# Kernel tuning notes

Hardware: AMD Instinct MI355X
Metric: run time of the kernel (lower is better)

## Reference

```python
import jax, jax.numpy as jnp
import numpy as np

DIM = 768
HEADS = 12
HEAD_DIM = DIM // HEADS
MLP_DIM = 4 * DIM
EPS = 1e-5


def setup_inputs() -> dict:
    key = jax.random.key(0)
    ks = jax.random.split(key, 8)
    s = lambda fan_in: 1.0 / np.sqrt(fan_in)
    return {
        "x": jax.random.normal(ks[0], (2, 2048, DIM), dtype=jnp.float32),
        "ln1_w": jnp.ones((DIM,), jnp.float32),
        "ln1_b": jnp.zeros((DIM,), jnp.float32),
        # weights stored [in, out]
        "qkv_w": jax.random.normal(ks[1], (DIM, 3 * DIM), jnp.float32) * s(DIM),
        "qkv_b": jnp.zeros((3 * DIM,), jnp.float32),
        "proj_w": jax.random.normal(ks[2], (DIM, DIM), jnp.float32) * s(DIM),
        "proj_b": jnp.zeros((DIM,), jnp.float32),
        "ln2_w": jnp.ones((DIM,), jnp.float32),
        "ln2_b": jnp.zeros((DIM,), jnp.float32),
        "lin1_w": jax.random.normal(ks[3], (DIM, MLP_DIM), jnp.float32) * s(DIM),
        "lin1_b": jnp.zeros((MLP_DIM,), jnp.float32),
        "lin2_w": jax.random.normal(ks[4], (MLP_DIM, DIM), jnp.float32) * s(MLP_DIM),
        "lin2_b": jnp.zeros((DIM,), jnp.float32),
    }


def _layernorm(x, w, b):
    mu = jnp.mean(x, axis=-1, keepdims=True)
    var = jnp.mean(jnp.square(x - mu), axis=-1, keepdims=True)
    return (x - mu) * jax.lax.rsqrt(var + EPS) * w + b


def _attention(x, qkv_w, qkv_b, proj_w, proj_b):
    B, N, C = x.shape
    qkv = (x @ qkv_w + qkv_b).reshape(B, N, 3, HEADS, HEAD_DIM)
    q, k, v = qkv[:, :, 0], qkv[:, :, 1], qkv[:, :, 2]  # [B, N, H, Dh]
    scale = HEAD_DIM ** -0.5
    attn = jnp.einsum("bqhd,bkhd->bhqk", q, k) * scale  # full NxN scores
    attn = jax.nn.softmax(attn, axis=-1)
    out = jnp.einsum("bhqk,bkhd->bqhd", attn, v).reshape(B, N, C)
    return out @ proj_w + proj_b


def reference(x, ln1_w, ln1_b, qkv_w, qkv_b, proj_w, proj_b,
              ln2_w, ln2_b, lin1_w, lin1_b, lin2_w, lin2_b):
    x = x + _attention(_layernorm(x, ln1_w, ln1_b), qkv_w, qkv_b, proj_w, proj_b)
    h = _layernorm(x, ln2_w, ln2_b)
    h = jax.nn.gelu(h @ lin1_w + lin1_b, approximate=False) @ lin2_w + lin2_b
    return x + h
```

## Files before the change

kernel.cpp:

```cpp
#include <hip/hip_runtime.h>
#include <hip/hip_bf16.h>
#include <math.h>

#define DIM 768
#define NTOK 4096
#define SEQ 2048
#define HEADS 12
#define HD 64

using bf16x8 = __attribute__((ext_vector_type(8))) __bf16;
using f32x4  = __attribute__((ext_vector_type(4))) float;
typedef unsigned short u16;

__device__ inline u16 f2bf(float f) {
  union { float f; unsigned u; } v; v.f = f;
  unsigned r = v.u + 0x7fffu + ((v.u >> 16) & 1u);
  return (u16)(r >> 16);
}

__device__ inline void pk2bf(float a, float b, u16* o0, u16* o1) {
  union { __hip_bfloat162 h; u16 u[2]; } cv;
  cv.h = __float22bfloat162_rn(make_float2(a, b));
  *o0 = cv.u[0];
  *o1 = cv.u[1];
}

__device__ inline unsigned pku32(float a, float b) {
  union { __hip_bfloat162 h; unsigned u; } cv;
  cv.h = __float22bfloat162_rn(make_float2(a, b));
  return cv.u;
}

__device__ inline void plane32_swap(unsigned &a, unsigned &b) {
  asm("v_permlane32_swap_b32 %0, %1" : "+v"(a), "+v"(b));
}
__device__ inline void plane16_swap(unsigned &a, unsigned &b) {
  asm("v_permlane16_swap_b32 %0, %1" : "+v"(a), "+v"(b));
}

__device__ inline float gelu_t(float x) {
  float z = x * (1.5957691216f + 0.0713548162f * x * x);
  return x / (1.0f + __expf(-z));
}

__device__ inline void gl_lds16(const u16* g, u16* l) {
  __builtin_amdgcn_global_load_lds(
      (const __attribute__((address_space(1))) unsigned int*)g,
      (__attribute__((address_space(3))) unsigned int*)l, 16, 0, 0);
}

__global__ __launch_bounds__(256) void ln_kernel(const float* __restrict__ x,
                                                 const float* __restrict__ w,
                                                 const float* __restrict__ b,
                                                 u16* __restrict__ y) {
  int row = blockIdx.x;
  int t = threadIdx.x;
  const float* xr = x + (size_t)row * DIM;
  float v0 = xr[t], v1 = xr[t + 256], v2 = xr[t + 512];
  float s = v0 + v1 + v2;
  float q = v0 * v0 + v1 * v1 + v2 * v2;
  for (int o = 32; o > 0; o >>= 1) {
    s += __shfl_down(s, o, 64);
    q += __shfl_down(q, o, 64);
  }
  __shared__ float ws_[4], wq_[4], mb[2];
  int wid = t >> 6;
  if ((t & 63) == 0) { ws_[wid] = s; wq_[wid] = q; }
  __syncthreads();
  if (t == 0) {
    float S = ws_[0] + ws_[1] + ws_[2] + ws_[3];
    float Q = wq_[0] + wq_[1] + wq_[2] + wq_[3];
    float mean = S * (1.0f / DIM);
    float var = Q * (1.0f / DIM) - mean * mean;
    mb[0] = mean;
    mb[1] = rsqrtf(var + 1e-5f);
  }
  __syncthreads();
  float mean = mb[0], rstd = mb[1];
  u16* yr = y + (size_t)row * DIM;
  yr[t]       = f2bf((v0 - mean) * rstd * w[t]       + b[t]);
  yr[t + 256] = f2bf((v1 - mean) * rstd * w[t + 256] + b[t + 256]);
  yr[t + 512] = f2bf((v2 - mean) * rstd * w[t + 512] + b[t + 512]);
}

__global__ __launch_bounds__(256) void redln_kernel(
    const float* __restrict__ P0, const float* __restrict__ P1,
    const float* __restrict__ bias, const float* __restrict__ res,
    float* __restrict__ x2, const float* __restrict__ lnw,
    const float* __restrict__ lnb, u16* __restrict__ y) {
  int row = blockIdx.x;
  int t = threadIdx.x;
  size_t off = (size_t)row * DIM;
  float v[3];
#pragma unroll
  for (int k = 0; k < 3; ++k) {
    int c = t + k * 256;
    v[k] = P0[off + c] + P1[off + c] + bias[c] + res[off + c];
    x2[off + c] = v[k];
  }
  float s = v[0] + v[1] + v[2];
  float q = v[0] * v[0] + v[1] * v[1] + v[2] * v[2];
  for (int o = 32; o > 0; o >>= 1) {
    s += __shfl_down(s, o, 64);
    q += __shfl_down(q, o, 64);
  }
  __shared__ float ws_[4], wq_[4], mb[2];
  int wid = t >> 6;
  if ((t & 63) == 0) { ws_[wid] = s; wq_[wid] = q; }
  __syncthreads();
  if (t == 0) {
    float S = ws_[0] + ws_[1] + ws_[2] + ws_[3];
    float Q = wq_[0] + wq_[1] + wq_[2] + wq_[3];
    float mean = S * (1.0f / DIM);
    float var = Q * (1.0f / DIM) - mean * mean;
    mb[0] = mean;
    mb[1] = rsqrtf(var + 1e-5f);
  }
  __syncthreads();
  float mean = mb[0], rstd = mb[1];
#pragma unroll
  for (int k = 0; k < 3; ++k) {
    int c = t + k * 256;
    y[off + c] = f2bf((v[k] - mean) * rstd * lnw[c] + lnb[c]);
  }
}

__global__ __launch_bounds__(256) void wcvt_all(
    const float* __restrict__ W0, const float* __restrict__ W1,
    const float* __restrict__ W2, const float* __restrict__ W3,
    u16* __restrict__ T0, u16* __restrict__ T1,
    u16* __restrict__ T2, u16* __restrict__ T3) {
  int id = blockIdx.x;
  const float* W; u16* Wt; int K, N, local;
  if (id < 1728)      { W = W0; Wt = T0; K = 768;  N = 2304; local = id; }
  else if (id < 2304) { W = W1; Wt = T1; K = 768;  N = 768;  local = id - 1728; }
  else if (id < 4608) { W = W2; Wt = T2; K = 768;  N = 3072; local = id - 2304; }
  else                { W = W3; Wt = T3; K = 3072; N = 768;  local = id - 4608; }
  int ntiles = N / 32;
  int n0 = (local % ntiles) * 32, k0 = (local / ntiles) * 32;
  __shared__ float tile[32][33];
  int tid = threadIdx.x;
  int c = tid & 31, r8 = tid >> 5;
#pragma unroll
  for (int p = 0; p < 4; ++p) {
    int k = r8 + p * 8;
    tile[k][c] = W[(size_t)(k0 + k) * N + n0 + c];
  }
  __syncthreads();
#pragma unroll
  for (int p = 0; p < 4; ++p) {
    int n = r8 + p * 8;
    Wt[(size_t)(n0 + n) * K + k0 + c] = f2bf(tile[c][n]);
  }
}

__global__ __launch_bounds__(256) void vtr_kernel(const u16* __restrict__ qkvB,
                                                  u16* __restrict__ vT) {
  __shared__ u16 tile[32][33];
  int v0 = blockIdx.x * 32, j0 = blockIdx.y * 32, b = blockIdx.z;
  int tid = threadIdx.x;
  int c = tid & 31, r8 = tid >> 5;
#pragma unroll
  for (int p = 0; p < 4; ++p) {
    int r = r8 + p * 8;
    tile[r][c] = qkvB[((size_t)(b * SEQ + j0 + r)) * 2304 + 1536 + v0 + c];
  }
  __syncthreads();
#pragma unroll
  for (int p = 0; p < 4; ++p) {
    int r = r8 + p * 8;
    vT[((size_t)(b * 768 + v0 + r)) * SEQ + j0 + c] = tile[c][r];
  }
}

__global__ __launch_bounds__(256) void bgemm_kernel(
    const u16* __restrict__ A, const u16* __restrict__ Bt,
    const float* __restrict__ bias, u16* __restrict__ Cb,
    int M, int N, int K, int act) {
  __shared__ __align__(16) u16 Asl[128 * 64];
  __shared__ __align__(16) u16 Bsl[128 * 64];
  int tid = threadIdx.x;
  int lane = tid & 63, wave = tid >> 6;
  int wm = wave >> 1, wn = wave & 1;
  int bm = blockIdx.y * 128, bn = blockIdx.x * 128;
  int l15 = lane & 15, quad = lane >> 4;
  int sm8 = tid >> 3;
  int kgx = (tid & 7) ^ (sm8 & 7);

  f32x4 acc[4][4] = {};
  const u16* Ap = A + (size_t)(bm + sm8) * K + kgx * 8;
  const u16* Bp = Bt + (size_t)(bn + sm8) * K + kgx * 8;
  u16* Al = &Asl[(wave * 8) * 64];
  u16* Bl = &Bsl[(wave * 8) * 64];
  int xr = l15 & 7;

  for (int k0 = 0; k0 < K; k0 += 64) {
#pragma unroll
    for (int p = 0; p < 4; ++p)
      gl_lds16(Ap + (size_t)(p * 32) * K + k0, Al + p * 32 * 64);
#pragma unroll
    for (int p = 0; p < 4; ++p)
      gl_lds16(Bp + (size_t)(p * 32) * K + k0, Bl + p * 32 * 64);
    __syncthreads();
#pragma unroll
    for (int ks = 0; ks < 2; ++ks) {
      int pu = ((ks << 2) + quad) ^ xr;
      bf16x8 af[4], bfr[4];
#pragma unroll
      for (int i = 0; i < 4; ++i) {
        af[i]  = *(const bf16x8*)&Asl[(wm * 64 + i * 16 + l15) * 64 + pu * 8];
        bfr[i] = *(const bf16x8*)&Bsl[(wn * 64 + i * 16 + l15) * 64 + pu * 8];
      }
#pragma unroll
      for (int i = 0; i < 4; ++i)
#pragma unroll
        for (int j = 0; j < 4; ++j)
          acc[i][j] = __builtin_amdgcn_mfma_f32_16x16x32_bf16(af[i], bfr[j], acc[i][j], 0, 0, 0);
    }
    __syncthreads();
  }

#pragma unroll
  for (int i = 0; i < 4; ++i) {
#pragma unroll
    for (int j = 0; j < 4; ++j) {
      int n = bn + wn * 64 + j * 16 + l15;
      float bv = bias[n];
      float val[4];
#pragma unroll
      for (int r = 0; r < 4; ++r) {
        float v = acc[i][j][r] + bv;
        val[r] = act ? gelu_t(v) : v;
      }
      u16 c0, c1, c2, c3;
      pk2bf(val[0], val[1], &c0, &c1);
      pk2bf(val[2], val[3], &c2, &c3);
      size_t mbase = (size_t)(bm + wm * 64 + i * 16 + quad * 4) * N + n;
      Cb[mbase]         = c0;
      Cb[mbase + N]     = c1;
      Cb[mbase + 2 * N] = c2;
      Cb[mbase + 3 * N] = c3;
    }
  }
}

__global__ __launch_bounds__(256) void bgemm_splitk(
    const u16* __restrict__ A, const u16* __restrict__ Bt,
    float* __restrict__ P0, float* __restrict__ P1,
    int M, int N, int K) {
  __shared__ __align__(16) u16 Asl[128 * 64];
  __shared__ __align__(16) u16 Bsl[64 * 64];
  int tid = threadIdx.x;
  int lane = tid & 63, wave = tid >> 6;
  int wm = wave >> 1, wn = wave & 1;
  int bm = blockIdx.y * 128, bn = blockIdx.x * 64;
  int l15 = lane & 15, quad = lane >> 4;
  int sm8 = tid >> 3;
  int kgx = (tid & 7) ^ (sm8 & 7);
  int half = K >> 1;
  int kbeg = blockIdx.z * half;

  f32x4 acc[4][2] = {};
  const u16* Ap = A + (size_t)(bm + sm8) * K + kbeg + kgx * 8;
  const u16* Bp = Bt + (size_t)(bn + sm8) * K + kbeg + kgx * 8;
  u16* Al = &Asl[(wave * 8) * 64];
  u16* Bl = &Bsl[(wave * 8) * 64];
  int xr = l15 & 7;

  for (int k0 = 0; k0 < half; k0 += 64) {
#pragma unroll
    for (int p = 0; p < 4; ++p)
      gl_lds16(Ap + (size_t)(p * 32) * K + k0, Al + p * 32 * 64);
#pragma unroll
    for (int p = 0; p < 2; ++p)
      gl_lds16(Bp + (size_t)(p * 32) * K + k0, Bl + p * 32 * 64);
    __syncthreads();
#pragma unroll
    for (int ks = 0; ks < 2; ++ks) {
      int pu = ((ks << 2) + quad) ^ xr;
      bf16x8 af[4], bfr[2];
#pragma unroll
      for (int i = 0; i < 4; ++i)
        af[i] = *(const bf16x8*)&Asl[(wm * 64 + i * 16 + l15) * 64 + pu * 8];
#pragma unroll
      for (int j = 0; j < 2; ++j)
        bfr[j] = *(const bf16x8*)&Bsl[(wn * 32 + j * 16 + l15) * 64 + pu * 8];
#pragma unroll
      for (int i = 0; i < 4; ++i)
#pragma unroll
        for (int j = 0; j < 2; ++j)
          acc[i][j] = __builtin_amdgcn_mfma_f32_16x16x32_bf16(af[i], bfr[j], acc[i][j], 0, 0, 0);
    }
    __syncthreads();
  }

  float* P = blockIdx.z ? P1 : P0;
#pragma unroll
  for (int i = 0; i < 4; ++i) {
#pragma unroll
    for (int j = 0; j < 2; ++j) {
      int n = bn + wn * 32 + j * 16 + l15;
#pragma unroll
      for (int r = 0; r < 4; ++r) {
        int m = bm + wm * 64 + i * 16 + quad * 4 + r;
        P[(size_t)m * N + n] = acc[i][j][r];
      }
    }
  }
}

__global__ __launch_bounds__(256) void red_kernel(
    const float* P0, const float* __restrict__ P1,
    const float* __restrict__ bias, const float* __restrict__ res,
    float* O, int Ncols) {
  int i = blockIdx.x * 256 + threadIdx.x;
  float4 a = ((const float4*)P0)[i];
  float4 b = ((const float4*)P1)[i];
  float4 r = ((const float4*)res)[i];
  int col = (i * 4) % Ncols;
  float4 bi = *(const float4*)&bias[col];
  float4 o;
  o.x = a.x + b.x + r.x + bi.x;
  o.y = a.y + b.y + r.y + bi.y;
  o.z = a.z + b.z + r.z + bi.z;
  o.w = a.w + b.w + r.w + bi.w;
  ((float4*)O)[i] = o;
}

__global__ __launch_bounds__(256) void attn_kernel(const u16* __restrict__ qkv,
                                                   const u16* __restrict__ vT,
                                                   u16* __restrict__ out) {
  __shared__ __align__(16) u16 Qs[64 * 64];
  __shared__ __align__(16) u16 Ks[2][64 * 64];
  __shared__ __align__(16) u16 Vs[2][64 * 64];

  int tid = threadIdx.x;
  int lane = tid & 63, wave = tid >> 6;
  int l15 = lane & 15, quad = lane >> 4;
  int qt = blockIdx.x * 64;
  int h = blockIdx.y, b = blockIdx.z;
  size_t base = (size_t)b * SEQ;
  int srow = lane >> 3;
  int sux = (lane & 7) ^ (srow & 7);
  int r0 = wave * 16;
  const u16* qbase = qkv + (base + qt) * 2304 + h * HD;
  const u16* kbase = qkv + base * 2304 + 768 + h * HD;
  const u16* vbase = vT + ((size_t)(b * HEADS + h) * HD) * SEQ;

  gl_lds16(qbase + (size_t)(r0 + srow) * 2304 + sux * 8, Qs + r0 * 64);
  gl_lds16(qbase + (size_t)(r0 + 8 + srow) * 2304 + sux * 8, Qs + (r0 + 8) * 64);
  gl_lds16(kbase + (size_t)(r0 + srow) * 2304 + sux * 8, Ks[0] + r0 * 64);
  gl_lds16(kbase + (size_t)(r0 + 8 + srow) * 2304 + sux * 8, Ks[0] + (r0 + 8) * 64);
  gl_lds16(vbase + (size_t)(r0 + srow) * SEQ + sux * 8, Vs[0] + r0 * 64);
  gl_lds16(vbase + (size_t)(r0 + 8 + srow) * SEQ + sux * 8, Vs[0] + (r0 + 8) * 64);
  __syncthreads();

  int xr = l15 & 7;
  bf16x8 aq0 = *(const bf16x8*)&Qs[(wave * 16 + l15) * 64 + ((quad ^ xr)) * 8];
  bf16x8 aq1 = *(const bf16x8*)&Qs[(wave * 16 + l15) * 64 + (((4 + quad) ^ xr)) * 8];

  f32x4 o_acc[4] = {};
  float lsum = 0.f;
  const float KEXP = 0.18033688011112042f;

  for (int t = 0; t < 32; ++t) {
    int buf = t & 1;
    if (t < 31) {
      size_t kt1 = (size_t)(t + 1) * 64;
      gl_lds16(kbase + (kt1 + r0 + srow) * 2304 + sux * 8, Ks[buf ^ 1] + r0 * 64);
      gl_lds16(kbase + (kt1 + r0 + 8 + srow) * 2304 + sux * 8, Ks[buf ^ 1] + (r0 + 8) * 64);
      gl_lds16(vbase + (size_t)(r0 + srow) * SEQ + kt1 + sux * 8, Vs[buf ^ 1] + r0 * 64);
      gl_lds16(vbase + (size_t)(r0 + 8 + srow) * SEQ + kt1 + sux * 8, Vs[buf ^ 1] + (r0 + 8) * 64);
    }

    f32x4 sT[4] = {};
    __builtin_amdgcn_s_setprio(1);
#pragma unroll
    for (int jt = 0; jt < 4; ++jt) {
      bf16x8 bk0 = *(const bf16x8*)&Ks[buf][(jt * 16 + l15) * 64 + ((quad ^ xr)) * 8];
      sT[jt] = __builtin_amdgcn_mfma_f32_16x16x32_bf16(bk0, aq0, sT[jt], 0, 0, 0);
      bf16x8 bk1 = *(const bf16x8*)&Ks[buf][(jt * 16 + l15) * 64 + (((4 + quad) ^ xr)) * 8];
      sT[jt] = __builtin_amdgcn_mfma_f32_16x16x32_bf16(bk1, aq1, sT[jt], 0, 0, 0);
    }
    __builtin_amdgcn_s_setprio(0);

    unsigned w01[4][2];
#pragma unroll
    for (int jt = 0; jt < 4; ++jt) {
      float p0 = __builtin_amdgcn_exp2f(sT[jt][0] * KEXP);
      float p1 = __builtin_amdgcn_exp2f(sT[jt][1] * KEXP);
      float p2 = __builtin_amdgcn_exp2f(sT[jt][2] * KEXP);
      float p3 = __builtin_amdgcn_exp2f(sT[jt][3] * KEXP);
      lsum += (p0 + p1) + (p2 + p3);
      w01[jt][0] = pku32(p0, p1);
      w01[jt][1] = pku32(p2, p3);
    }

    __builtin_amdgcn_s_setprio(1);
#pragma unroll
    for (int ks = 0; ks < 2; ++ks) {
      unsigned a0 = w01[2 * ks][0], b0 = w01[2 * ks + 1][0];
      plane32_swap(a0, b0);
      plane16_swap(a0, b0);
      unsigned a1 = w01[2 * ks][1], b1 = w01[2 * ks + 1][1];
      plane32_swap(a1, b1);
      plane16_swap(a1, b1);
      union { bf16x8 v; unsigned u[4]; } AP;
      AP.u[0] = a0; AP.u[1] = a1; AP.u[2] = b0; AP.u[3] = b1;
#pragma unroll
      for (int dt = 0; dt < 4; ++dt) {
        bf16x8 bv = *(const bf16x8*)&Vs[buf][(dt * 16 + l15) * 64 + (((ks << 2) + quad) ^ xr) * 8];
        o_acc[dt] = __builtin_amdgcn_mfma_f32_16x16x32_bf16(AP.v, bv, o_acc[dt], 0, 0, 0);
      }
    }
    __builtin_amdgcn_s_setprio(0);
    __syncthreads();
  }

  lsum += __shfl_xor(lsum, 16, 64);
  lsum += __shfl_xor(lsum, 32, 64);
  float linv = 1.0f / lsum;
  float lr[4];
#pragma unroll
  for (int r = 0; r < 4; ++r) lr[r] = __shfl(linv, quad * 4 + r, 64);

#pragma unroll
  for (int r = 0; r < 4; ++r) {
    size_t trow = (base + qt + wave * 16 + quad * 4 + r) * DIM + h * HD;
    u16 c0, c1, c2, c3;
    pk2bf(o_acc[0][r] * lr[r], o_acc[1][r] * lr[r], &c0, &c1);
    pk2bf(o_acc[2][r] * lr[r], o_acc[3][r] * lr[r], &c2, &c3);
    out[trow + 0 * 16 + l15] = c0;
    out[trow + 1 * 16 + l15] = c1;
    out[trow + 2 * 16 + l15] = c2;
    out[trow + 3 * 16 + l15] = c3;
  }
}

extern "C" void kernel_launch(void* const* d_in, const int* in_sizes, int n_in,
                              void* d_out, int out_size, void* d_ws, size_t ws_size,
                              hipStream_t stream) {
  const float* x     = (const float*)d_in[0];
  const float* ln1w  = (const float*)d_in[1];
  const float* ln1b  = (const float*)d_in[2];
  const float* qkvw  = (const float*)d_in[3];
  const float* qkvbi = (const float*)d_in[4];
  const float* projw = (const float*)d_in[5];
  const float* projb = (const float*)d_in[6];
  const float* ln2w  = (const float*)d_in[7];
  const float* ln2b  = (const float*)d_in[8];
  const float* l1w   = (const float*)d_in[9];
  const float* l1b   = (const float*)d_in[10];
  const float* l2w   = (const float*)d_in[11];
  const float* l2b   = (const float*)d_in[12];
  float* out = (float*)d_out;

  char* w = (char*)d_ws;
  u16*   h     = (u16*)w;   w += (size_t)NTOK * DIM * 2;
  u16*   qkvB  = (u16*)w;
  u16*   mid   = (u16*)w;   w += (size_t)NTOK * 3072 * 2;
  u16*   attnb = (u16*)w;   w += (size_t)NTOK * DIM * 2;
  float* x2    = (float*)w; w += (size_t)NTOK * DIM * 4;
  u16*   vTb   = (u16*)w;   w += (size_t)NTOK * DIM * 2;
  u16*   qkvwt = (u16*)w;   w += (size_t)DIM * 2304 * 2;
  u16*   projwt= (u16*)w;   w += (size_t)DIM * DIM * 2;
  u16*   l1wt  = (u16*)w;   w += (size_t)DIM * 3072 * 2;
  u16*   l2wt  = (u16*)w;   w += (size_t)3072 * DIM * 2;
  float* Pbuf  = (float*)w; w += (size_t)NTOK * DIM * 4;

  wcvt_all<<<6912, 256, 0, stream>>>(qkvw, projw, l1w, l2w,
                                     qkvwt, projwt, l1wt, l2wt);

  ln_kernel<<<NTOK, 256, 0, stream>>>(x, ln1w, ln1b, h);
  bgemm_kernel<<<dim3(2304 / 128, NTOK / 128), 256, 0, stream>>>(
      h, qkvwt, qkvbi, qkvB, NTOK, 2304, DIM, 0);
  vtr_kernel<<<dim3(768 / 32, SEQ / 32, 2), 256, 0, stream>>>(qkvB, vTb);
  attn_kernel<<<dim3(SEQ / 64, HEADS, 2), 256, 0, stream>>>(qkvB, vTb, attnb);

  bgemm_splitk<<<dim3(DIM / 64, NTOK / 128, 2), 256, 0, stream>>>(
      attnb, projwt, x2, Pbuf, NTOK, DIM, DIM);
  redln_kernel<<<NTOK, 256, 0, stream>>>(x2, Pbuf, projb, x, x2, ln2w, ln2b, h);

  bgemm_kernel<<<dim3(3072 / 128, NTOK / 128), 256, 0, stream>>>(
      h, l1wt, l1b, mid, NTOK, 3072, DIM, 1);

  bgemm_splitk<<<dim3(DIM / 64, NTOK / 128, 2), 256, 0, stream>>>(
      mid, l2wt, out, Pbuf, NTOK, DIM, 3072);
  red_kernel<<<NTOK * DIM / 1024, 256, 0, stream>>>(out, Pbuf, l2b, x2, out, DIM);
}
```

Before: 279.0 us.

## Split attention work across waves by key rows with cross-wave LDS reduction

The attention kernel's work is repartitioned. Each wave now owns 16 of the 64 key rows in every tile and computes scores against all 64 queries, held in registers. P@V uses 16x16x16 MFMAs taking P directly from the score accumulator layout, which removes the permlane swaps. Partial outputs and row sums are reduced across the four waves through LDS at the end, and the launch bounds ask for 3 blocks per SM. In exchange there are more accumulator registers (16 f32x4), an extra LDS reduction phase with several syncs, and half-width MFMAs for the PV product.

```diff
diff --git a/kernel.cpp b/kernel.cpp
--- a/kernel.cpp
+++ b/kernel.cpp
@@ -9,6 +9,8 @@
 #define HD 64
 
 using bf16x8 = __attribute__((ext_vector_type(8))) __bf16;
+using bf16x4 = __attribute__((ext_vector_type(4))) __bf16;
+using short4v = __attribute__((ext_vector_type(4))) short;
 using f32x4  = __attribute__((ext_vector_type(4))) float;
 typedef unsigned short u16;
 
@@ -29,13 +31,6 @@
   union { __hip_bfloat162 h; unsigned u; } cv;
   cv.h = __float22bfloat162_rn(make_float2(a, b));
   return cv.u;
-}
-
-__device__ inline void plane32_swap(unsigned &a, unsigned &b) {
-  asm("v_permlane32_swap_b32 %0, %1" : "+v"(a), "+v"(b));
-}
-__device__ inline void plane16_swap(unsigned &a, unsigned &b) {
-  asm("v_permlane16_swap_b32 %0, %1" : "+v"(a), "+v"(b));
 }
 
 __device__ inline float gelu_t(float x) {
@@ -327,12 +322,14 @@
   ((float4*)O)[i] = o;
 }
 
-__global__ __launch_bounds__(256) void attn_kernel(const u16* __restrict__ qkv,
-                                                   const u16* __restrict__ vT,
-                                                   u16* __restrict__ out) {
-  __shared__ __align__(16) u16 Qs[64 * 64];
-  __shared__ __align__(16) u16 Ks[2][64 * 64];
-  __shared__ __align__(16) u16 Vs[2][64 * 64];
+#define LDP 68
+__global__ __launch_bounds__(256, 3) void attn_kernel(const u16* __restrict__ qkv,
+                                                      const u16* __restrict__ vT,
+                                                      u16* __restrict__ out) {
+  __shared__ __align__(16) char arena[40960];
+  u16* Qsp = (u16*)arena;
+  u16* Ksp = (u16*)(arena + 8192);
+  u16* Vsp = (u16*)(arena + 24576);
 
   int tid = threadIdx.x;
   int lane = tid & 63, wave = tid >> 6;
@@ -347,93 +344,130 @@
   const u16* kbase = qkv + base * 2304 + 768 + h * HD;
   const u16* vbase = vT + ((size_t)(b * HEADS + h) * HD) * SEQ;
 
-  gl_lds16(qbase + (size_t)(r0 + srow) * 2304 + sux * 8, Qs + r0 * 64);
-  gl_lds16(qbase + (size_t)(r0 + 8 + srow) * 2304 + sux * 8, Qs + (r0 + 8) * 64);
-  gl_lds16(kbase + (size_t)(r0 + srow) * 2304 + sux * 8, Ks[0] + r0 * 64);
-  gl_lds16(kbase + (size_t)(r0 + 8 + srow) * 2304 + sux * 8, Ks[0] + (r0 + 8) * 64);
-  gl_lds16(vbase + (size_t)(r0 + srow) * SEQ + sux * 8, Vs[0] + r0 * 64);
-  gl_lds16(vbase + (size_t)(r0 + 8 + srow) * SEQ + sux * 8, Vs[0] + (r0 + 8) * 64);
+  gl_lds16(qbase + (size_t)(r0 + srow) * 2304 + sux * 8, Qsp + r0 * 64);
+  gl_lds16(qbase + (size_t)(r0 + 8 + srow) * 2304 + sux * 8, Qsp + (r0 + 8) * 64);
+  gl_lds16(kbase + (size_t)(r0 + srow) * 2304 + sux * 8, Ksp + r0 * 64);
+  gl_lds16(kbase + (size_t)(r0 + 8 + srow) * 2304 + sux * 8, Ksp + (r0 + 8) * 64);
+  gl_lds16(vbase + (size_t)(r0 + srow) * SEQ + sux * 8, Vsp + r0 * 64);
+  gl_lds16(vbase + (size_t)(r0 + 8 + srow) * SEQ + sux * 8, Vsp + (r0 + 8) * 64);
   __syncthreads();
 
   int xr = l15 & 7;
-  bf16x8 aq0 = *(const bf16x8*)&Qs[(wave * 16 + l15) * 64 + ((quad ^ xr)) * 8];
-  bf16x8 aq1 = *(const bf16x8*)&Qs[(wave * 16 + l15) * 64 + (((4 + quad) ^ xr)) * 8];
-
-  f32x4 o_acc[4] = {};
-  float lsum = 0.f;
+  bf16x8 qf[4][2];
+#pragma unroll
+  for (int g = 0; g < 4; ++g)
+#pragma unroll
+    for (int s = 0; s < 2; ++s)
+      qf[g][s] = *(const bf16x8*)&Qsp[(g * 16 + l15) * 64 + ((s * 4 + quad) ^ xr) * 8];
+
+  int koff0 = (wave * 16 + l15) * 64 + ((quad ^ xr)) * 8;
+  int koff1 = (wave * 16 + l15) * 64 + (((4 + quad) ^ xr)) * 8;
+  int voff[4];
+#pragma unroll
+  for (int dg = 0; dg < 4; ++dg)
+    voff[dg] = (dg * 16 + l15) * 64 + (((2 * wave + (quad >> 1)) ^ xr)) * 8 + (quad & 1) * 4;
+
+  f32x4 oT[4][4] = {};
+  float lsum[4] = {0.f, 0.f, 0.f, 0.f};
   const float KEXP = 0.18033688011112042f;
 
   for (int t = 0; t < 32; ++t) {
     int buf = t & 1;
     if (t < 31) {
       size_t kt1 = (size_t)(t + 1) * 64;
-      gl_lds16(kbase + (kt1 + r0 + srow) * 2304 + sux * 8, Ks[buf ^ 1] + r0 * 64);
-      gl_lds16(kbase + (kt1 + r0 + 8 + srow) * 2304 + sux * 8, Ks[buf ^ 1] + (r0 + 8) * 64);
-      gl_lds16(vbase + (size_t)(r0 + srow) * SEQ + kt1 + sux * 8, Vs[buf ^ 1] + r0 * 64);
-      gl_lds16(vbase + (size_t)(r0 + 8 + srow) * SEQ + kt1 + sux * 8, Vs[buf ^ 1] + (r0 + 8) * 64);
-    }
+      u16* Kd = Ksp + (buf ^ 1) * 4096;
+      u16* Vd = Vsp + (buf ^ 1) * 4096;
+      gl_lds16(kbase + (kt1 + r0 + srow) * 2304 + sux * 8, Kd + r0 * 64);
+      gl_lds16(kbase + (kt1 + r0 + 8 + srow) * 2304 + sux * 8, Kd + (r0 + 8) * 64);
+      gl_lds16(vbase + (size_t)(r0 + srow) * SEQ + kt1 + sux * 8, Vd + r0 * 64);
+      gl_lds16(vbase + (size_t)(r0 + 8 + srow) * SEQ + kt1 + sux * 8, Vd + (r0 + 8) * 64);
+    }
+    const u16* Kb = Ksp + buf * 4096;
+    const u16* Vb = Vsp + buf * 4096;
 
     f32x4 sT[4] = {};
     __builtin_amdgcn_s_setprio(1);
-#pragma unroll
-    for (int jt = 0; jt < 4; ++jt) {
-      bf16x8 bk0 = *(const bf16x8*)&Ks[buf][(jt * 16 + l15) * 64 + ((quad ^ xr)) * 8];
-      sT[jt] = __builtin_amdgcn_mfma_f32_16x16x32_bf16(bk0, aq0, sT[jt], 0, 0, 0);
-      bf16x8 bk1 = *(const bf16x8*)&Ks[buf][(jt * 16 + l15) * 64 + (((4 + quad) ^ xr)) * 8];
-      sT[jt] = __builtin_amdgcn_mfma_f32_16x16x32_bf16(bk1, aq1, sT[jt], 0, 0, 0);
+    {
+      bf16x8 ak = *(const bf16x8*)&Kb[koff0];
+#pragma unroll
+      for (int g = 0; g < 4; ++g)
+        sT[g] = __builtin_amdgcn_mfma_f32_16x16x32_bf16(ak, qf[g][0], sT[g], 0, 0, 0);
+      bf16x8 ak1 = *(const bf16x8*)&Kb[koff1];
+#pragma unroll
+      for (int g = 0; g < 4; ++g)
+        sT[g] = __builtin_amdgcn_mfma_f32_16x16x32_bf16(ak1, qf[g][1], sT[g], 0, 0, 0);
     }
     __builtin_amdgcn_s_setprio(0);
 
-    unsigned w01[4][2];
-#pragma unroll
-    for (int jt = 0; jt < 4; ++jt) {
-      float p0 = __builtin_amdgcn_exp2f(sT[jt][0] * KEXP);
-      float p1 = __builtin_amdgcn_exp2f(sT[jt][1] * KEXP);
-      float p2 = __builtin_amdgcn_exp2f(sT[jt][2] * KEXP);
-      float p3 = __builtin_amdgcn_exp2f(sT[jt][3] * KEXP);
-      lsum += (p0 + p1) + (p2 + p3);
-      w01[jt][0] = pku32(p0, p1);
-      w01[jt][1] = pku32(p2, p3);
-    }
-
+    short4v pb[4];
+#pragma unroll
+    for (int g = 0; g < 4; ++g) {
+      float p0 = __builtin_amdgcn_exp2f(sT[g][0] * KEXP);
+      float p1 = __builtin_amdgcn_exp2f(sT[g][1] * KEXP);
+      float p2 = __builtin_amdgcn_exp2f(sT[g][2] * KEXP);
+      float p3 = __builtin_amdgcn_exp2f(sT[g][3] * KEXP);
+      lsum[g] += (p0 + p1) + (p2 + p3);
+      union { unsigned u[2]; short4v s; } cv;
+      cv.u[0] = pku32(p0, p1);
+      cv.u[1] = pku32(p2, p3);
+      pb[g] = cv.s;
+    }
+
+    short4v av[4];
+#pragma unroll
+    for (int dg = 0; dg < 4; ++dg)
+      av[dg] = *(const short4v*)&Vb[voff[dg]];
     __builtin_amdgcn_s_setprio(1);
 #pragma unroll
-    for (int ks = 0; ks < 2; ++ks) {
-      unsigned a0 = w01[2 * ks][0], b0 = w01[2 * ks + 1][0];
-      plane32_swap(a0, b0);
-      plane16_swap(a0, b0);
-      unsigned a1 = w01[2 * ks][1], b1 = w01[2 * ks + 1][1];
-      plane32_swap(a1, b1);
-      plane16_swap(a1, b1);
-      union { bf16x8 v; unsigned u[4]; } AP;
-      AP.u[0] = a0; AP.u[1] = a1; AP.u[2] = b0; AP.u[3] = b1;
-#pragma unroll
-      for (int dt = 0; dt < 4; ++dt) {
-        bf16x8 bv = *(const bf16x8*)&Vs[buf][(dt * 16 + l15) * 64 + (((ks << 2) + quad) ^ xr) * 8];
-        o_acc[dt] = __builtin_amdgcn_mfma_f32_16x16x32_bf16(AP.v, bv, o_acc[dt], 0, 0, 0);
-      }
-    }
+    for (int dg = 0; dg < 4; ++dg)
+#pragma unroll
+      for (int g = 0; g < 4; ++g)
+        oT[dg][g] = __builtin_amdgcn_mfma_f32_16x16x16bf16_1k(av[dg], pb[g], oT[dg][g], 0, 0, 0);
     __builtin_amdgcn_s_setprio(0);
     __syncthreads();
   }
 
-  lsum += __shfl_xor(lsum, 16, 64);
-  lsum += __shfl_xor(lsum, 32, 64);
-  float linv = 1.0f / lsum;
-  float lr[4];
-#pragma unroll
-  for (int r = 0; r < 4; ++r) lr[r] = __shfl(linv, quad * 4 + r, 64);
-
-#pragma unroll
-  for (int r = 0; r < 4; ++r) {
-    size_t trow = (base + qt + wave * 16 + quad * 4 + r) * DIM + h * HD;
-    u16 c0, c1, c2, c3;
-    pk2bf(o_acc[0][r] * lr[r], o_acc[1][r] * lr[r], &c0, &c1);
-    pk2bf(o_acc[2][r] * lr[r], o_acc[3][r] * lr[r], &c2, &c3);
-    out[trow + 0 * 16 + l15] = c0;
-    out[trow + 1 * 16 + l15] = c1;
-    out[trow + 2 * 16 + l15] = c2;
-    out[trow + 3 * 16 + l15] = c3;
+#pragma unroll
+  for (int g = 0; g < 4; ++g) {
+    lsum[g] += __shfl_xor(lsum[g], 16, 64);
+    lsum[g] += __shfl_xor(lsum[g], 32, 64);
+  }
+  float* LDSw = (float*)arena;
+  float* lsd  = (float*)(arena + 17408);
+  if (lane < 16) {
+#pragma unroll
+    for (int g = 0; g < 4; ++g) lsd[wave * 64 + g * 16 + lane] = lsum[g];
+  }
+  float linv = 0.f;
+#pragma unroll
+  for (int dg = 0; dg < 4; ++dg) {
+#pragma unroll
+    for (int g = 0; g < 4; ++g)
+#pragma unroll
+      for (int r = 0; r < 4; ++r)
+        LDSw[wave * (16 * LDP) + (quad * 4 + r) * LDP + g * 16 + l15] = oT[dg][g][r];
+    __syncthreads();
+    if (dg == 0) {
+      float L = lsd[wave * 16 + l15] + lsd[64 + wave * 16 + l15] +
+                lsd[128 + wave * 16 + l15] + lsd[192 + wave * 16 + l15];
+      linv = 1.0f / L;
+    }
+    float sv[4];
+#pragma unroll
+    for (int i = 0; i < 4; ++i) {
+      int dloc = quad * 4 + i;
+      float a = LDSw[dloc * LDP + wave * 16 + l15] +
+                LDSw[1 * (16 * LDP) + dloc * LDP + wave * 16 + l15] +
+                LDSw[2 * (16 * LDP) + dloc * LDP + wave * 16 + l15] +
+                LDSw[3 * (16 * LDP) + dloc * LDP + wave * 16 + l15];
+      sv[i] = a * linv;
+    }
+    size_t addr = (base + qt + wave * 16 + l15) * DIM + h * HD + dg * 16 + quad * 4;
+    uint2 pk;
+    pk.x = pku32(sv[0], sv[1]);
+    pk.y = pku32(sv[2], sv[3]);
+    *(uint2*)&out[addr] = pk;
+    __syncthreads();
   }
 }
 
```

Measured after the change: 278.8 us. About the same (-0.1%).
